# Performance work log

Hardware: AMD Instinct MI355X
Metric: run time of the kernel (lower is better)

## Reference

```python
import jax, jax.numpy as jnp
import numpy as np

B, T, H = 128, 512, 512  # batch, max timesteps, hidden (= input_size = output_size)


def setup_inputs() -> dict:
    key = jax.random.key(0)
    k1, k2, k3, k4 = jax.random.split(key, 4)
    x = jax.random.normal(k1, (B, T, H), dtype=jnp.float32)
    scale = 1.0 / np.sqrt(H)
    # torch.nn.Linear default init: U(-1/sqrt(fan_in), 1/sqrt(fan_in))
    W_in = jax.random.uniform(k2, (H, 6 * H), minval=-scale, maxval=scale, dtype=jnp.float32)
    b_in = jax.random.uniform(k3, (6 * H,), minval=-scale, maxval=scale, dtype=jnp.float32)
    # PackedSequence semantics: lengths sorted descending, longest == T
    lengths = jax.random.randint(k4, (B,), 1, T + 1)
    lengths = jnp.sort(lengths)[::-1].at[0].set(T).astype(jnp.int64)
    return {"x": x, "lengths": lengths, "W_in": W_in, "b_in": b_in}


def reference(x, lengths, W_in, b_in):
    # Faithful to the source: input_linearity is applied to BOTH the timestep
    # input and the previous state (the module never uses state_linearity in
    # forward). The ragged batch slicing [0:current_length_index+1] combined
    # with re-zeroing the full-batch state each step is exactly equivalent to
    # masking with (t < lengths) for sorted-descending lengths.
    Bx, Tx, _ = x.shape
    Hs = W_in.shape[0]
    proj_x = jnp.einsum('bti,io->bto', x, W_in) + b_in  # [B,T,6H], hoisted out of the loop

    def step(carry, inp):
        h, c = carry
        px, t = inp  # px: [B,6H]
        g = px + (h @ W_in + b_in)  # projected_input + projected_state
        i = jax.nn.sigmoid(g[:, 0 * Hs:1 * Hs])
        f = jax.nn.sigmoid(g[:, 1 * Hs:2 * Hs])
        m = jnp.tanh(g[:, 2 * Hs:3 * Hs])
        o = jax.nn.sigmoid(g[:, 3 * Hs:4 * Hs])
        c_new = i * m + f * c
        out = o * jnp.tanh(c_new)
        hw = jax.nn.sigmoid(g[:, 4 * Hs:5 * Hs])
        out = hw * out + (1.0 - hw) * px[:, 5 * Hs:6 * Hs]  # highway proj uses input only
        active = (t < lengths)[:, None]  # [B,1]
        h_new = jnp.where(active, out, 0.0)
        c_new = jnp.where(active, c_new, 0.0)
        return (h_new, c_new), h_new

    init = (jnp.zeros((Bx, Hs), x.dtype), jnp.zeros((Bx, Hs), x.dtype))
    _, ys = jax.lax.scan(step, init, (proj_x.transpose(1, 0, 2), jnp.arange(Tx)))
    return ys.transpose(1, 0, 2)  # [B,T,H], zero past each sequence length
```

## Files before the change

kernel.cpp:

```cpp
#include <hip/hip_runtime.h>
#include <hip/hip_bf16.h>

#define Tz 512
#define Hz 512
#define NG 8
#define BG 16
#define SL 16
#define NWAVE 6
#define NTHR (NWAVE * 64)
#define SIXH (6 * Hz)
#define HB_U32 (BG * Hz)
#define WS_U32 (2 * NG * HB_U32)

typedef __bf16 bf16x8 __attribute__((ext_vector_type(8)));
typedef float f32x4 __attribute__((ext_vector_type(4)));
typedef unsigned int u32;
typedef u32 u32x4v __attribute__((ext_vector_type(4)));

__device__ __forceinline__ u32x4v ld_coh_x4(const u32* p) {
  u32x4v r;
  asm volatile("global_load_dwordx4 %0, %1, off sc0 sc1" : "=v"(r) : "v"(p) : "memory");
  return r;
}
__device__ __forceinline__ void st_coh_u32(u32* p, u32 v) {
  asm volatile("global_store_dword %0, %1, off sc0 sc1" :: "v"(p), "v"(v) : "memory");
}
__device__ __forceinline__ void vm_wait0() {
  asm volatile("s_waitcnt vmcnt(0)" ::: "memory");
  __builtin_amdgcn_sched_barrier(0);
}
__device__ __forceinline__ float sigf(float x) { return 1.f / (1.f + __expf(-x)); }
__device__ __forceinline__ float tanh_f(float x) { return 2.f / (1.f + __expf(-2.f * x)) - 1.f; }
__device__ __forceinline__ u32 pk_bf16(float a, float b) {
  unsigned short lo = __builtin_bit_cast(unsigned short, (__bf16)a);
  unsigned short hi = __builtin_bit_cast(unsigned short, (__bf16)b);
  return (u32)lo | ((u32)hi << 16);
}

__global__ void lstm_init(u32* ws) {
  int i = blockIdx.x * blockDim.x + threadIdx.x;
  ws[i] = 0xFFFF0000u;
}

__global__ __launch_bounds__(NTHR) void lstm_main(
    const float* __restrict__ x, const int* __restrict__ lens,
    const float* __restrict__ Wg, const float* __restrict__ bg,
    float* __restrict__ out, u32* __restrict__ hb)
{
  const int tid = threadIdx.x;
  const int l   = tid & 63;
  const int w   = tid >> 6;
  const int wg  = blockIdx.x;
  const int gi  = wg & 7;
  const int si  = wg >> 3;
  const int oct = l >> 4;
  const int lm  = l & 15;

  __shared__ __align__(16) char xs[2][BG * Hz * 2];
  __shared__ __align__(16) char hs[BG * Hz * 2];
  __shared__ float gs[NWAVE][BG][SL];

  const int colg = w * Hz + si * SL + lm;
  bf16x8 wf[16];
#pragma unroll
  for (int s = 0; s < 16; ++s) {
#pragma unroll
    for (int j = 0; j < 8; ++j) {
      wf[s][j] = (__bf16)Wg[(size_t)(32 * s + 8 * oct + j) * SIXH + colg];
    }
  }
  const float bv = bg[colg];
  const float bias = (w < 5) ? 2.f * bv : bv;

  const int erow = tid >> 4;
  const int ecol = tid & 15;
  float cc = 0.f;
  int mylen = 0;
  if (tid < 256) mylen = lens[gi * BG + erow];

  float4 f[8];

  if (tid < 256) {
    const float4* xr = (const float4*)(x + ((size_t)(gi * BG + erow) * Tz + 0) * Hz + ecol * 32);
    float4 f0[8];
#pragma unroll
    for (int q = 0; q < 8; ++q) f0[q] = xr[q];
#pragma unroll
    for (int Q = 0; Q < 4; ++Q) {
      u32x4v v = { pk_bf16(f0[2*Q].x, f0[2*Q].y),   pk_bf16(f0[2*Q].z, f0[2*Q].w),
                   pk_bf16(f0[2*Q+1].x, f0[2*Q+1].y), pk_bf16(f0[2*Q+1].z, f0[2*Q+1].w) };
      int byte = (erow * 1024 + ecol * 64 + 16 * Q) ^ ((erow & 7) << 4);
      *(u32x4v*)(&xs[0][byte]) = v;
    }
    const float4* xr1 = (const float4*)(x + ((size_t)(gi * BG + erow) * Tz + 1) * Hz + ecol * 32);
#pragma unroll
    for (int q = 0; q < 8; ++q) f[q] = xr1[q];
  }
  __syncthreads();

  for (int t = 0; t < Tz; ++t) {
    const bool do_h = (t > 0) && (tid < 256);
    const u32* hp = hb + ((size_t)((t + 1) & 1) * NG + gi) * HB_U32 + erow * Hz + ecol * 32;
    u32x4v hv4[8];
    if (do_h) {
#pragma unroll
      for (int q = 0; q < 8; ++q) hv4[q] = ld_coh_x4(hp + 4 * q);
    }
    f32x4 acc0; acc0[0] = bias; acc0[1] = bias; acc0[2] = bias; acc0[3] = bias;
    f32x4 acc1; acc1[0] = 0.f; acc1[1] = 0.f; acc1[2] = 0.f; acc1[3] = 0.f;
    {
      const char* xb = xs[t & 1];
#pragma unroll
      for (int s = 0; s < 16; ++s) {
        int byte = (lm * 1024 + 64 * s + 16 * oct) ^ ((lm & 7) << 4);
        bf16x8 a = *(const bf16x8*)(xb + byte);
        if (s & 1) acc1 = __builtin_amdgcn_mfma_f32_16x16x32_bf16(a, wf[s], acc1, 0, 0, 0);
        else       acc0 = __builtin_amdgcn_mfma_f32_16x16x32_bf16(a, wf[s], acc0, 0, 0, 0);
      }
    }
    if (tid < 256) vm_wait0();
    if (do_h) {
      const u32 etag = (u32)(t - 1);
      u32 badmask = 0;
#pragma unroll
      for (int q = 0; q < 8; ++q) {
        bool b = false;
#pragma unroll
        for (int j = 0; j < 4; ++j) b |= ((hv4[q][j] >> 16) != etag);
        badmask |= (u32)b << q;
      }
      int guard = 0;
      while (__builtin_expect(badmask != 0, 0)) {
#pragma unroll
        for (int q = 0; q < 8; ++q)
          if (badmask & (1u << q)) hv4[q] = ld_coh_x4(hp + 4 * q);
        vm_wait0();
        u32 nb = 0;
#pragma unroll
        for (int q = 0; q < 8; ++q) {
          bool b = false;
#pragma unroll
          for (int j = 0; j < 4; ++j) b |= ((hv4[q][j] >> 16) != etag);
          nb |= (u32)b << q;
        }
        badmask = nb;
        if (++guard > 1000000) break;
      }
#pragma unroll
      for (int k2 = 0; k2 < 4; ++k2) {
        u32x4v o;
#pragma unroll
        for (int m = 0; m < 4; ++m) {
          int c = 8 * k2 + 2 * m;
          o[m] = __builtin_amdgcn_perm(hv4[(c + 1) >> 2][(c + 1) & 3],
                                       hv4[c >> 2][c & 3], 0x05040100u);
        }
        int byte = (erow * 1024 + ecol * 64 + 16 * k2) ^ ((erow & 7) << 4);
        *(u32x4v*)(&hs[byte]) = o;
      }
    }
    if (tid < 256 && t + 1 < Tz) {
#pragma unroll
      for (int Q = 0; Q < 4; ++Q) {
        u32x4v v = { pk_bf16(f[2*Q].x, f[2*Q].y),   pk_bf16(f[2*Q].z, f[2*Q].w),
                     pk_bf16(f[2*Q+1].x, f[2*Q+1].y), pk_bf16(f[2*Q+1].z, f[2*Q+1].w) };
        int byte = (erow * 1024 + ecol * 64 + 16 * Q) ^ ((erow & 7) << 4);
        *(u32x4v*)(&xs[(t + 1) & 1][byte]) = v;
      }
      if (t + 2 < Tz) {
        const float4* xr = (const float4*)(x + ((size_t)(gi * BG + erow) * Tz + (t + 2)) * Hz + ecol * 32);
#pragma unroll
        for (int q = 0; q < 8; ++q) f[q] = xr[q];
      }
    }
    __syncthreads();
    if (w < 5 && t > 0) {
#pragma unroll
      for (int s = 0; s < 16; ++s) {
        int byte = (lm * 1024 + 64 * s + 16 * oct) ^ ((lm & 7) << 4);
        bf16x8 a = *(const bf16x8*)(hs + byte);
        if (s & 1) acc1 = __builtin_amdgcn_mfma_f32_16x16x32_bf16(a, wf[s], acc1, 0, 0, 0);
        else       acc0 = __builtin_amdgcn_mfma_f32_16x16x32_bf16(a, wf[s], acc0, 0, 0, 0);
      }
    }
    {
      f32x4 g = acc0 + acc1;
#pragma unroll
      for (int r = 0; r < 4; ++r) gs[w][oct * 4 + r][lm] = g[r];
    }
    __syncthreads();
    if (tid < 256) {
      float g0 = gs[0][erow][ecol], g1 = gs[1][erow][ecol], g2 = gs[2][erow][ecol];
      float g3 = gs[3][erow][ecol], g4 = gs[4][erow][ecol], px5 = gs[5][erow][ecol];
      float ig = sigf(g0), fg = sigf(g1), mg = tanh_f(g2), og = sigf(g3), hg = sigf(g4);
      float cn = ig * mg + fg * cc;
      float ot = og * tanh_f(cn);
      ot = hg * ot + (1.f - hg) * px5;
      bool act = t < mylen;
      float hv = act ? ot : 0.f;
      cc = act ? cn : 0.f;
      u32 tagged = ((u32)t << 16) | (u32)__builtin_bit_cast(unsigned short, (__bf16)hv);
      u32* hwp = hb + ((size_t)(t & 1) * NG + gi) * HB_U32 + erow * Hz + si * SL + ecol;
      st_coh_u32(hwp, tagged);
      out[((size_t)(gi * BG + erow) * Tz + t) * Hz + si * SL + ecol] = hv;
    }
  }
}

extern "C" void kernel_launch(void* const* d_in, const int* in_sizes, int n_in,
                              void* d_out, int out_size, void* d_ws, size_t ws_size,
                              hipStream_t stream) {
  const float* x  = (const float*)d_in[0];
  const int* lens = (const int*)d_in[1];
  const float* Wg = (const float*)d_in[2];
  const float* bg = (const float*)d_in[3];
  float* out = (float*)d_out;
  u32* hb = (u32*)d_ws;

  hipLaunchKernelGGL(lstm_init, dim3(WS_U32 / 256), dim3(256), 0, stream, hb);
  hipLaunchKernelGGL(lstm_main, dim3(256), dim3(NTHR), 0, stream,
                     x, lens, Wg, bg, out, hb);
}
```

Before: 2.310 ms.

## Process two batch groups per workgroup with interleaved steps, halving grid size

Each workgroup now handles two batch groups (A and B) for the same column slice, so the grid drops from 256 to 128 workgroups. Register-resident weight fragments are reused across both groups, and group B's processing, including its global handshake wait, overlaps with group A's work. This halves the number of cross-workgroup participants and doubles per-workgroup LDS and register use. The cost is a longer per-step critical path, since each workgroup does twice the MFMA and elementwise work serially, and the added registers may cause spills.

Result: slower. 3.762 ms (+62.8%).

```diff
diff --git a/kernel.cpp b/kernel.cpp
--- a/kernel.cpp
+++ b/kernel.cpp
@@ -51,14 +51,15 @@
   const int l   = tid & 63;
   const int w   = tid >> 6;
   const int wg  = blockIdx.x;
-  const int gi  = wg & 7;
-  const int si  = wg >> 3;
+  const int pr  = wg & 3;
+  const int si  = wg >> 2;
+  const int giA = 2 * pr, giB = 2 * pr + 1;
   const int oct = l >> 4;
   const int lm  = l & 15;
 
-  __shared__ __align__(16) char xs[2][BG * Hz * 2];
-  __shared__ __align__(16) char hs[BG * Hz * 2];
-  __shared__ float gs[NWAVE][BG][SL];
+  __shared__ __align__(16) char xs[2][2][BG * Hz * 2];
+  __shared__ __align__(16) char hs[2][BG * Hz * 2];
+  __shared__ float gs[2][NWAVE][BG][SL];
 
   const int colg = w * Hz + si * SL + lm;
   bf16x8 wf[16];
@@ -74,73 +75,60 @@
 
   const int erow = tid >> 4;
   const int ecol = tid & 15;
-  float cc = 0.f;
-  int mylen = 0;
-  if (tid < 256) mylen = lens[gi * BG + erow];
-
-  float4 f[8];
+  float ccA = 0.f, ccB = 0.f;
+  int lenA = 0, lenB = 0;
+  if (tid < 256) { lenA = lens[giA * BG + erow]; lenB = lens[giB * BG + erow]; }
+
+  float4 fA[8], fB[8];
 
   if (tid < 256) {
-    const float4* xr = (const float4*)(x + ((size_t)(gi * BG + erow) * Tz + 0) * Hz + ecol * 32);
-    float4 f0[8];
-#pragma unroll
-    for (int q = 0; q < 8; ++q) f0[q] = xr[q];
-#pragma unroll
-    for (int Q = 0; Q < 4; ++Q) {
-      u32x4v v = { pk_bf16(f0[2*Q].x, f0[2*Q].y),   pk_bf16(f0[2*Q].z, f0[2*Q].w),
-                   pk_bf16(f0[2*Q+1].x, f0[2*Q+1].y), pk_bf16(f0[2*Q+1].z, f0[2*Q+1].w) };
-      int byte = (erow * 1024 + ecol * 64 + 16 * Q) ^ ((erow & 7) << 4);
-      *(u32x4v*)(&xs[0][byte]) = v;
-    }
-    const float4* xr1 = (const float4*)(x + ((size_t)(gi * BG + erow) * Tz + 1) * Hz + ecol * 32);
-#pragma unroll
-    for (int q = 0; q < 8; ++q) f[q] = xr1[q];
+#pragma unroll
+    for (int G = 0; G < 2; ++G) {
+      const int gi = G ? giB : giA;
+      const float4* xr = (const float4*)(x + ((size_t)(gi * BG + erow) * Tz + 0) * Hz + ecol * 32);
+      float4 f0[8];
+#pragma unroll
+      for (int q = 0; q < 8; ++q) f0[q] = xr[q];
+#pragma unroll
+      for (int Q = 0; Q < 4; ++Q) {
+        u32x4v v = { pk_bf16(f0[2*Q].x, f0[2*Q].y),   pk_bf16(f0[2*Q].z, f0[2*Q].w),
+                     pk_bf16(f0[2*Q+1].x, f0[2*Q+1].y), pk_bf16(f0[2*Q+1].z, f0[2*Q+1].w) };
+        int byte = (erow * 1024 + ecol * 64 + 16 * Q) ^ ((erow & 7) << 4);
+        *(u32x4v*)(&xs[G][0][byte]) = v;
+      }
+    }
+    const float4* xa = (const float4*)(x + ((size_t)(giA * BG + erow) * Tz + 1) * Hz + ecol * 32);
+    const float4* xb = (const float4*)(x + ((size_t)(giB * BG + erow) * Tz + 1) * Hz + ecol * 32);
+#pragma unroll
+    for (int q = 0; q < 8; ++q) { fA[q] = xa[q]; fB[q] = xb[q]; }
   }
   __syncthreads();
 
-  for (int t = 0; t < Tz; ++t) {
-    const bool do_h = (t > 0) && (tid < 256);
-    const u32* hp = hb + ((size_t)((t + 1) & 1) * NG + gi) * HB_U32 + erow * Hz + ecol * 32;
-    u32x4v hv4[8];
-    if (do_h) {
-#pragma unroll
-      for (int q = 0; q < 8; ++q) hv4[q] = ld_coh_x4(hp + 4 * q);
-    }
-    f32x4 acc0; acc0[0] = bias; acc0[1] = bias; acc0[2] = bias; acc0[3] = bias;
-    f32x4 acc1; acc1[0] = 0.f; acc1[1] = 0.f; acc1[2] = 0.f; acc1[3] = 0.f;
-    {
-      const char* xb = xs[t & 1];
-#pragma unroll
-      for (int s = 0; s < 16; ++s) {
-        int byte = (lm * 1024 + 64 * s + 16 * oct) ^ ((lm & 7) << 4);
-        bf16x8 a = *(const bf16x8*)(xb + byte);
-        if (s & 1) acc1 = __builtin_amdgcn_mfma_f32_16x16x32_bf16(a, wf[s], acc1, 0, 0, 0);
-        else       acc0 = __builtin_amdgcn_mfma_f32_16x16x32_bf16(a, wf[s], acc0, 0, 0, 0);
-      }
-    }
-    if (tid < 256) vm_wait0();
-    if (do_h) {
+  auto process = [&](const int G, const int gi, const u32* hp, u32x4v* hv,
+                     float4* fx, f32x4& a0, f32x4& a1, float& cc,
+                     const int len, const int t) {
+    if (t > 0 && tid < 256) {
       const u32 etag = (u32)(t - 1);
       u32 badmask = 0;
 #pragma unroll
       for (int q = 0; q < 8; ++q) {
         bool b = false;
 #pragma unroll
-        for (int j = 0; j < 4; ++j) b |= ((hv4[q][j] >> 16) != etag);
+        for (int j = 0; j < 4; ++j) b |= ((hv[q][j] >> 16) != etag);
         badmask |= (u32)b << q;
       }
       int guard = 0;
       while (__builtin_expect(badmask != 0, 0)) {
 #pragma unroll
         for (int q = 0; q < 8; ++q)
-          if (badmask & (1u << q)) hv4[q] = ld_coh_x4(hp + 4 * q);
+          if (badmask & (1u << q)) hv[q] = ld_coh_x4(hp + 4 * q);
         vm_wait0();
         u32 nb = 0;
 #pragma unroll
         for (int q = 0; q < 8; ++q) {
           bool b = false;
 #pragma unroll
-          for (int j = 0; j < 4; ++j) b |= ((hv4[q][j] >> 16) != etag);
+          for (int j = 0; j < 4; ++j) b |= ((hv[q][j] >> 16) != etag);
           nb |= (u32)b << q;
         }
         badmask = nb;
@@ -152,25 +140,25 @@
 #pragma unroll
         for (int m = 0; m < 4; ++m) {
           int c = 8 * k2 + 2 * m;
-          o[m] = __builtin_amdgcn_perm(hv4[(c + 1) >> 2][(c + 1) & 3],
-                                       hv4[c >> 2][c & 3], 0x05040100u);
+          o[m] = __builtin_amdgcn_perm(hv[(c + 1) >> 2][(c + 1) & 3],
+                                       hv[c >> 2][c & 3], 0x05040100u);
         }
         int byte = (erow * 1024 + ecol * 64 + 16 * k2) ^ ((erow & 7) << 4);
-        *(u32x4v*)(&hs[byte]) = o;
+        *(u32x4v*)(&hs[G][byte]) = o;
       }
     }
     if (tid < 256 && t + 1 < Tz) {
 #pragma unroll
       for (int Q = 0; Q < 4; ++Q) {
-        u32x4v v = { pk_bf16(f[2*Q].x, f[2*Q].y),   pk_bf16(f[2*Q].z, f[2*Q].w),
-                     pk_bf16(f[2*Q+1].x, f[2*Q+1].y), pk_bf16(f[2*Q+1].z, f[2*Q+1].w) };
+        u32x4v v = { pk_bf16(fx[2*Q].x, fx[2*Q].y),   pk_bf16(fx[2*Q].z, fx[2*Q].w),
+                     pk_bf16(fx[2*Q+1].x, fx[2*Q+1].y), pk_bf16(fx[2*Q+1].z, fx[2*Q+1].w) };
         int byte = (erow * 1024 + ecol * 64 + 16 * Q) ^ ((erow & 7) << 4);
-        *(u32x4v*)(&xs[(t + 1) & 1][byte]) = v;
+        *(u32x4v*)(&xs[G][(t + 1) & 1][byte]) = v;
       }
       if (t + 2 < Tz) {
         const float4* xr = (const float4*)(x + ((size_t)(gi * BG + erow) * Tz + (t + 2)) * Hz + ecol * 32);
 #pragma unroll
-        for (int q = 0; q < 8; ++q) f[q] = xr[q];
+        for (int q = 0; q < 8; ++q) fx[q] = xr[q];
       }
     }
     __syncthreads();
@@ -178,32 +166,63 @@
 #pragma unroll
       for (int s = 0; s < 16; ++s) {
         int byte = (lm * 1024 + 64 * s + 16 * oct) ^ ((lm & 7) << 4);
-        bf16x8 a = *(const bf16x8*)(hs + byte);
-        if (s & 1) acc1 = __builtin_amdgcn_mfma_f32_16x16x32_bf16(a, wf[s], acc1, 0, 0, 0);
-        else       acc0 = __builtin_amdgcn_mfma_f32_16x16x32_bf16(a, wf[s], acc0, 0, 0, 0);
+        bf16x8 a = *(const bf16x8*)(hs[G] + byte);
+        if (s & 1) a1 = __builtin_amdgcn_mfma_f32_16x16x32_bf16(a, wf[s], a1, 0, 0, 0);
+        else       a0 = __builtin_amdgcn_mfma_f32_16x16x32_bf16(a, wf[s], a0, 0, 0, 0);
       }
     }
     {
-      f32x4 g = acc0 + acc1;
-#pragma unroll
-      for (int r = 0; r < 4; ++r) gs[w][oct * 4 + r][lm] = g[r];
+      f32x4 g = a0 + a1;
+#pragma unroll
+      for (int r = 0; r < 4; ++r) gs[G][w][oct * 4 + r][lm] = g[r];
     }
     __syncthreads();
     if (tid < 256) {
-      float g0 = gs[0][erow][ecol], g1 = gs[1][erow][ecol], g2 = gs[2][erow][ecol];
-      float g3 = gs[3][erow][ecol], g4 = gs[4][erow][ecol], px5 = gs[5][erow][ecol];
+      float g0 = gs[G][0][erow][ecol], g1 = gs[G][1][erow][ecol], g2 = gs[G][2][erow][ecol];
+      float g3 = gs[G][3][erow][ecol], g4 = gs[G][4][erow][ecol], px5 = gs[G][5][erow][ecol];
       float ig = sigf(g0), fg = sigf(g1), mg = tanh_f(g2), og = sigf(g3), hg = sigf(g4);
       float cn = ig * mg + fg * cc;
       float ot = og * tanh_f(cn);
       ot = hg * ot + (1.f - hg) * px5;
-      bool act = t < mylen;
-      float hv = act ? ot : 0.f;
+      bool act = t < len;
+      float hv2 = act ? ot : 0.f;
       cc = act ? cn : 0.f;
-      u32 tagged = ((u32)t << 16) | (u32)__builtin_bit_cast(unsigned short, (__bf16)hv);
+      u32 tagged = ((u32)t << 16) | (u32)__builtin_bit_cast(unsigned short, (__bf16)hv2);
       u32* hwp = hb + ((size_t)(t & 1) * NG + gi) * HB_U32 + erow * Hz + si * SL + ecol;
       st_coh_u32(hwp, tagged);
-      out[((size_t)(gi * BG + erow) * Tz + t) * Hz + si * SL + ecol] = hv;
-    }
+      out[((size_t)(gi * BG + erow) * Tz + t) * Hz + si * SL + ecol] = hv2;
+    }
+  };
+
+  for (int t = 0; t < Tz; ++t) {
+    const bool do_h = (t > 0) && (tid < 256);
+    const u32* hpA = hb + ((size_t)((t + 1) & 1) * NG + giA) * HB_U32 + erow * Hz + ecol * 32;
+    const u32* hpB = hb + ((size_t)((t + 1) & 1) * NG + giB) * HB_U32 + erow * Hz + ecol * 32;
+    u32x4v hA[8], hB[8];
+    if (do_h) {
+#pragma unroll
+      for (int q = 0; q < 8; ++q) hB[q] = ld_coh_x4(hpB + 4 * q);
+#pragma unroll
+      for (int q = 0; q < 8; ++q) hA[q] = ld_coh_x4(hpA + 4 * q);
+    }
+    f32x4 aA0, aA1, aB0, aB1;
+    aA0[0]=bias; aA0[1]=bias; aA0[2]=bias; aA0[3]=bias;
+    aB0[0]=bias; aB0[1]=bias; aB0[2]=bias; aB0[3]=bias;
+    aA1[0]=0.f; aA1[1]=0.f; aA1[2]=0.f; aA1[3]=0.f;
+    aB1[0]=0.f; aB1[1]=0.f; aB1[2]=0.f; aB1[3]=0.f;
+#pragma unroll
+    for (int s = 0; s < 16; ++s) {
+      int byte = (lm * 1024 + 64 * s + 16 * oct) ^ ((lm & 7) << 4);
+      bf16x8 aB = *(const bf16x8*)(xs[1][t & 1] + byte);
+      bf16x8 aA = *(const bf16x8*)(xs[0][t & 1] + byte);
+      if (s & 1) { aB1 = __builtin_amdgcn_mfma_f32_16x16x32_bf16(aB, wf[s], aB1, 0, 0, 0);
+                   aA1 = __builtin_amdgcn_mfma_f32_16x16x32_bf16(aA, wf[s], aA1, 0, 0, 0); }
+      else       { aB0 = __builtin_amdgcn_mfma_f32_16x16x32_bf16(aB, wf[s], aB0, 0, 0, 0);
+                   aA0 = __builtin_amdgcn_mfma_f32_16x16x32_bf16(aA, wf[s], aA0, 0, 0, 0); }
+    }
+    if (tid < 256) vm_wait0();
+    process(1, giB, hpB, hB, fB, aB0, aB1, ccB, lenB, t);
+    process(0, giA, hpA, hA, fA, aA0, aA1, ccA, lenA, t);
   }
 }
 
@@ -218,6 +237,6 @@
   u32* hb = (u32*)d_ws;
 
   hipLaunchKernelGGL(lstm_init, dim3(WS_U32 / 256), dim3(256), 0, stream, hb);
-  hipLaunchKernelGGL(lstm_main, dim3(256), dim3(NTHR), 0, stream,
+  hipLaunchKernelGGL(lstm_main, dim3(128), dim3(NTHR), 0, stream,
                      x, lens, Wg, bg, out, hb);
 }
```
